# Kernel tuning notes

Measured on AMD Instinct MI355X. Metric: run time of the kernel, lower is better.

Reference implementation:

```python
import jax, jax.numpy as jnp
import numpy as np

N_NODES = 50000
N_EDGES = 800000
IN, HID, OUT = 128, 32, 64
HEADS = (4, 4, 4, 4)  # heads per layer (heads[0], heads[1], heads[1], heads[2])
NEG_SLOPE = 0.2


def gat_layer(h, src, dst, W, al, ar, b, activation):
    """One DGL-style GATConv. h: [N, Din]; W: [Din, H*F]; al, ar: [H, F]; b: [H*F]."""
    n = h.shape[0]
    H, F = al.shape
    feat = (h @ W).reshape(n, H, F)                       # [N, H, F]
    el = jnp.sum(feat * al, axis=-1)                      # [N, H]
    er = jnp.sum(feat * ar, axis=-1)                      # [N, H]
    e = jax.nn.leaky_relu(el[src] + er[dst], NEG_SLOPE)   # [E, H]
    # segment softmax over incoming edges of each dst node
    m = jax.ops.segment_max(e, dst, num_segments=n)       # [N, H]
    ex = jnp.exp(e - m[dst])                              # [E, H]
    denom = jax.ops.segment_sum(ex, dst, num_segments=n)  # [N, H]
    alpha = ex / jnp.maximum(denom[dst], 1e-9)            # [E, H]
    msg = feat[src] * alpha[:, :, None]                   # [E, H, F]
    out = jax.ops.segment_sum(msg, dst, num_segments=n) + b.reshape(H, F)
    return activation(out) if activation is not None else out


def setup_inputs() -> dict:
    key = jax.random.key(0)
    ks = jax.random.split(key, 20)
    x = jax.random.normal(ks[0], (N_NODES, IN), dtype=jnp.float32)
    src = jax.random.randint(ks[1], (N_EDGES,), 0, N_NODES, dtype=jnp.int32)
    dst = jax.random.randint(ks[2], (N_EDGES,), 0, N_NODES, dtype=jnp.int32)
    dims = [(IN, HEADS[0], HID), (HID * HEADS[0], HEADS[1], HID),
            (HID * HEADS[1], HEADS[2], HID), (HID * HEADS[2], HEADS[3], OUT)]
    inp = {"x": x, "src": src, "dst": dst}
    k = 3
    for i, (din, h, f) in enumerate(dims, start=1):
        inp[f"W{i}"] = jax.random.normal(ks[k], (din, h * f), dtype=jnp.float32) * 0.05; k += 1
        inp[f"al{i}"] = jax.random.normal(ks[k], (h, f), dtype=jnp.float32) * 0.05; k += 1
        inp[f"ar{i}"] = jax.random.normal(ks[k], (h, f), dtype=jnp.float32) * 0.05; k += 1
        inp[f"b{i}"] = jnp.zeros((h * f,), dtype=jnp.float32)
    return inp


def reference(x, src, dst, W1, al1, ar1, b1, W2, al2, ar2, b2,
              W3, al3, ar3, b3, W4, al4, ar4, b4):
    elu = jax.nn.elu
    h = gat_layer(x, src, dst, W1, al1, ar1, b1, elu).reshape(N_NODES, -1)   # flatten heads
    h = gat_layer(h, src, dst, W2, al2, ar2, b2, elu).reshape(N_NODES, -1)
    h = gat_layer(h, src, dst, W3, al3, ar3, b3, elu).reshape(N_NODES, -1)
    h = gat_layer(h, src, dst, W4, al4, ar4, b4, None).mean(axis=1)          # mean over heads
    return h
```

## Files before the change

### kernel.cpp

```cpp
#include <hip/hip_runtime.h>
#include <hip/hip_fp16.h>

#define N_NODES 50000
#define N_EDGES 800000

typedef _Float16 h8 __attribute__((ext_vector_type(8)));
typedef float f4 __attribute__((ext_vector_type(4)));

__device__ __forceinline__ float lrelu(float x){ return x > 0.f ? x : 0.2f*x; }
__device__ __forceinline__ float eluf (float x){ return x > 0.f ? x : __expf(x)-1.f; }

__global__ void k_histwt(const int* __restrict__ dst, int* __restrict__ cnt,
                         const float* __restrict__ W1, const float* __restrict__ W2,
                         const float* __restrict__ W3, const float* __restrict__ W4,
                         _Float16* __restrict__ wt){
  int b = blockIdx.x;
  if (b < 3125){
    int e = b*256 + threadIdx.x;
    if (e < N_EDGES) atomicAdd(&cnt[dst[e]], 1);
  } else {
    int id = (b - 3125)*256 + threadIdx.x;
    if (id < 81920){
      const float* W; int HF; int loc;
      if (id < 16384)      { W = W1; HF = 128; loc = id; }
      else if (id < 32768) { W = W2; HF = 128; loc = id - 16384; }
      else if (id < 49152) { W = W3; HF = 128; loc = id - 32768; }
      else                 { W = W4; HF = 256; loc = id - 49152; }
      int n = loc >> 7, k = loc & 127;
      wt[id] = (_Float16)W[(size_t)k*HF + n];
    }
  }
}

__global__ void k_scan1(const int* __restrict__ cnt, int* __restrict__ offs, int* __restrict__ bsum){
  __shared__ int tmp[256];
  int tid = threadIdx.x; int i = blockIdx.x*256 + tid;
  int v = (i < N_NODES) ? cnt[i] : 0;
  tmp[tid] = v; __syncthreads();
  for (int d = 1; d < 256; d <<= 1){
    int t = (tid >= d) ? tmp[tid-d] : 0;
    __syncthreads();
    tmp[tid] += t;
    __syncthreads();
  }
  if (i < N_NODES) offs[i] = tmp[tid] - v;
  if (tid == 255) bsum[blockIdx.x] = tmp[tid];
}

__global__ void k_scan2(int* __restrict__ bsum, int nb){
  __shared__ int tmp[256];
  int tid = threadIdx.x;
  int v = (tid < nb) ? bsum[tid] : 0;
  tmp[tid] = v; __syncthreads();
  for (int d = 1; d < 256; d <<= 1){
    int t = (tid >= d) ? tmp[tid-d] : 0;
    __syncthreads();
    tmp[tid] += t;
    __syncthreads();
  }
  if (tid < nb) bsum[tid] = tmp[tid] - v;
}

__global__ void k_scan3(int* __restrict__ offs, const int* __restrict__ bsum, int* __restrict__ cur){
  int i = blockIdx.x*256 + threadIdx.x;
  if (i < N_NODES){
    int o = offs[i] + bsum[blockIdx.x];
    offs[i] = o; cur[i] = o;
  }
  if (i == 0) offs[N_NODES] = N_EDGES;
}

__global__ void k_scatter(const int* __restrict__ src, const int* __restrict__ dst,
                          int* __restrict__ cur, int* __restrict__ csr_src){
  int e = blockIdx.x*256 + threadIdx.x;
  if (e < N_EDGES){
    int pos = atomicAdd(&cur[dst[e]], 1);
    csr_src[pos] = src[e];
  }
}

template<int HF, bool AHALF>
__global__ __launch_bounds__(256) void k_gemm(const void* __restrict__ Ain,
        const _Float16* __restrict__ Wt,
        __half* __restrict__ feat,
        const float* __restrict__ al, const float* __restrict__ ar,
        float* __restrict__ el, float* __restrict__ er){
  __shared__ char lds[49152];
  char* Alds = lds;
  char* Blds = lds + 32768;
  _Float16* Clds = (_Float16*)lds;
  const int tid  = threadIdx.x;
  const int row0 = blockIdx.x * 128;
  const int col0 = blockIdx.y * 64;

  if (AHALF){
    const __half* A16 = (const __half*)Ain;
    #pragma unroll
    for (int i = 0; i < 8; ++i){
      int flat = i*256 + tid;
      int r = flat >> 4, ch = flat & 15;
      uint4 v = make_uint4(0,0,0,0);
      if (row0 + r < N_NODES) v = *(const uint4*)&A16[(size_t)(row0+r)*128 + ch*8];
      *(uint4*)(Alds + ((r*256 + ch*16) ^ ((r&7)<<4))) = v;
    }
  } else {
    const float* A32 = (const float*)Ain;
    #pragma unroll
    for (int i = 0; i < 8; ++i){
      int flat = i*256 + tid;
      int r = flat >> 4, ch = flat & 15;
      h8 hv = {};
      if (row0 + r < N_NODES){
        float4 f0 = *(const float4*)&A32[(size_t)(row0+r)*128 + ch*8];
        float4 f1 = *(const float4*)&A32[(size_t)(row0+r)*128 + ch*8 + 4];
        hv[0]=(_Float16)f0.x; hv[1]=(_Float16)f0.y; hv[2]=(_Float16)f0.z; hv[3]=(_Float16)f0.w;
        hv[4]=(_Float16)f1.x; hv[5]=(_Float16)f1.y; hv[6]=(_Float16)f1.z; hv[7]=(_Float16)f1.w;
      }
      *(h8*)(Alds + ((r*256 + ch*16) ^ ((r&7)<<4))) = hv;
    }
  }
  #pragma unroll
  for (int i = 0; i < 4; ++i){
    int flat = i*256 + tid;
    int n = flat >> 4, ch = flat & 15;
    uint4 v = *(const uint4*)&Wt[(size_t)(col0+n)*128 + ch*8];
    *(uint4*)(Blds + ((n*256 + ch*16) ^ ((n&7)<<4))) = v;
  }
  __syncthreads();

  const int l = tid & 63, w = tid >> 6;
  f4 acc[2][4] = {};
  const int rA0  = w*32 + (l & 15);
  const int rA1  = rA0 + 16;
  const int nB   = (l & 15);
  const int ksel = (l >> 4) * 16;
  #pragma unroll
  for (int kb = 0; kb < 4; ++kb){
    int kofs = kb*64 + ksel;
    h8 a0 = *(const h8*)(Alds + ((rA0*256 + kofs) ^ ((rA0&7)<<4)));
    h8 a1 = *(const h8*)(Alds + ((rA1*256 + kofs) ^ ((rA1&7)<<4)));
    h8 b[4];
    #pragma unroll
    for (int nf = 0; nf < 4; ++nf){
      int n = nB + nf*16;
      b[nf] = *(const h8*)(Blds + ((n*256 + kofs) ^ ((n&7)<<4)));
    }
    #pragma unroll
    for (int nf = 0; nf < 4; ++nf){
      acc[0][nf] = __builtin_amdgcn_mfma_f32_16x16x32_f16(a0, b[nf], acc[0][nf], 0, 0, 0);
      acc[1][nf] = __builtin_amdgcn_mfma_f32_16x16x32_f16(a1, b[nf], acc[1][nf], 0, 0, 0);
    }
  }
  __syncthreads();

  #pragma unroll
  for (int mf = 0; mf < 2; ++mf){
    int rloc = w*32 + mf*16 + (l>>4)*4;
    #pragma unroll
    for (int nf = 0; nf < 4; ++nf){
      int c = nf*16 + (l&15);
      #pragma unroll
      for (int reg = 0; reg < 4; ++reg)
        Clds[(rloc+reg)*80 + c] = (_Float16)acc[mf][nf][reg];
    }
  }
  __syncthreads();

  constexpr int F = HF/4;
  int ch = l & 7;
  float4 al0 = *(const float4*)&al[col0 + ch*8];
  float4 al1 = *(const float4*)&al[col0 + ch*8 + 4];
  float4 ar0 = *(const float4*)&ar[col0 + ch*8];
  float4 ar1 = *(const float4*)&ar[col0 + ch*8 + 4];
  #pragma unroll
  for (int i = 0; i < 4; ++i){
    int rloc = i*32 + w*8 + (l>>3);
    int grow = row0 + rloc;
    h8 hv = *(const h8*)&Clds[rloc*80 + ch*8];
    if (grow < N_NODES)
      *(uint4*)&feat[(size_t)grow*HF + col0 + ch*8] = *(uint4*)&hv;
    float f0=(float)hv[0], f1=(float)hv[1], f2=(float)hv[2], f3=(float)hv[3];
    float f4_=(float)hv[4], f5=(float)hv[5], f6=(float)hv[6], f7=(float)hv[7];
    float pl = f0*al0.x + f1*al0.y + f2*al0.z + f3*al0.w
             + f4_*al1.x + f5*al1.y + f6*al1.z + f7*al1.w;
    float pr = f0*ar0.x + f1*ar0.y + f2*ar0.z + f3*ar0.w
             + f4_*ar1.x + f5*ar1.y + f6*ar1.z + f7*ar1.w;
    pl += __shfl_xor(pl, 1); pl += __shfl_xor(pl, 2);
    pr += __shfl_xor(pr, 1); pr += __shfl_xor(pr, 2);
    if (F == 64){ pl += __shfl_xor(pl, 4); pr += __shfl_xor(pr, 4); }
    bool lead = (F == 32) ? ((l & 3) == 0) : ((l & 7) == 0);
    if (lead && grow < N_NODES){
      int h = (col0 + ch*8) / F;
      el[grow*4 + h] = pl;
      er[grow*4 + h] = pr;
    }
  }
}

template<int F, bool FINAL, int LAYER>
__global__ __launch_bounds__(256) void k_agg(const int* __restrict__ offs,
        const int* __restrict__ csr_src, const float* __restrict__ el,
        const float* __restrict__ er, const __half* __restrict__ feat,
        const float* __restrict__ bias, void* __restrict__ out){
  __shared__ float s_ev[4][64][4];
  __shared__ int   s_src[4][64];
  int tid  = threadIdx.x;
  int wv   = tid >> 6;
  int lane = tid & 63;
  int n = blockIdx.x*4 + wv;
  int beg = offs[n], end = offs[n+1];
  float4 er4 = ((const float4*)er)[n];

  if (F == 32){
    int quarter = lane >> 4;
    int l4      = lane & 15;
    int h       = l4 >> 2;
    float a0=0.f,a1=0.f,a2=0.f,a3=0.f,a4=0.f,a5=0.f,a6=0.f,a7=0.f,ds=0.f;
    for (int cbeg = beg; cbeg < end; cbeg += 64){
      int m = end - cbeg; if (m > 64) m = 64;
      if (lane < m){
        int s = csr_src[cbeg + lane];
        s_src[wv][lane] = s;
        float4 e4 = *(const float4*)&el[(size_t)s*4];
        float4 ev4;
        ev4.x = __expf(lrelu(e4.x + er4.x));
        ev4.y = __expf(lrelu(e4.y + er4.y));
        ev4.z = __expf(lrelu(e4.z + er4.z));
        ev4.w = __expf(lrelu(e4.w + er4.w));
        *(float4*)&s_ev[wv][lane][0] = ev4;
      }
      asm volatile("s_waitcnt lgkmcnt(0)" ::: "memory");
      #pragma unroll 4
      for (int i = 0; i < m; i += 4){
        int e = i + quarter;
        if (e < m){
          int s = s_src[wv][e];
          float w = s_ev[wv][e][h];
          ds += w;
          uint4 raw = *(const uint4*)&feat[(size_t)s*128 + l4*8];
          const __half2* hp = reinterpret_cast<const __half2*>(&raw);
          float2 f0 = __half22float2(hp[0]);
          float2 f1 = __half22float2(hp[1]);
          float2 f2 = __half22float2(hp[2]);
          float2 f3 = __half22float2(hp[3]);
          a0 += w*f0.x; a1 += w*f0.y; a2 += w*f1.x; a3 += w*f1.y;
          a4 += w*f2.x; a5 += w*f2.y; a6 += w*f3.x; a7 += w*f3.y;
        }
      }
      asm volatile("" ::: "memory");
    }
    ds += __shfl_xor(ds, 16); ds += __shfl_xor(ds, 32);
    a0 += __shfl_xor(a0, 16); a0 += __shfl_xor(a0, 32);
    a1 += __shfl_xor(a1, 16); a1 += __shfl_xor(a1, 32);
    a2 += __shfl_xor(a2, 16); a2 += __shfl_xor(a2, 32);
    a3 += __shfl_xor(a3, 16); a3 += __shfl_xor(a3, 32);
    a4 += __shfl_xor(a4, 16); a4 += __shfl_xor(a4, 32);
    a5 += __shfl_xor(a5, 16); a5 += __shfl_xor(a5, 32);
    a6 += __shfl_xor(a6, 16); a6 += __shfl_xor(a6, 32);
    a7 += __shfl_xor(a7, 16); a7 += __shfl_xor(a7, 32);
    if (quarter == 0){
      float rden = 1.f / fmaxf(ds, 1e-9f);
      float4 b0 = *(const float4*)&bias[l4*8];
      float4 b1 = *(const float4*)&bias[l4*8 + 4];
      float o0 = eluf(a0*rden + b0.x);
      float o1 = eluf(a1*rden + b0.y);
      float o2 = eluf(a2*rden + b0.z);
      float o3 = eluf(a3*rden + b0.w);
      float o4 = eluf(a4*rden + b1.x);
      float o5 = eluf(a5*rden + b1.y);
      float o6 = eluf(a6*rden + b1.z);
      float o7 = eluf(a7*rden + b1.w);
      __half* outh = (__half*)out;
      h8 hv;
      hv[0]=(_Float16)o0; hv[1]=(_Float16)o1; hv[2]=(_Float16)o2; hv[3]=(_Float16)o3;
      hv[4]=(_Float16)o4; hv[5]=(_Float16)o5; hv[6]=(_Float16)o6; hv[7]=(_Float16)o7;
      *(uint4*)&outh[(size_t)n*128 + l4*8] = *(uint4*)&hv;
    }
  } else {
    int hw  = lane >> 5;
    int l5  = lane & 31;
    int h   = l5 >> 3;
    float a0=0.f,a1=0.f,a2=0.f,a3=0.f,a4=0.f,a5=0.f,a6=0.f,a7=0.f,ds=0.f;
    for (int cbeg = beg; cbeg < end; cbeg += 64){
      int m = end - cbeg; if (m > 64) m = 64;
      if (lane < m){
        int s = csr_src[cbeg + lane];
        s_src[wv][lane] = s;
        float4 e4 = *(const float4*)&el[(size_t)s*4];
        float4 ev4;
        ev4.x = __expf(lrelu(e4.x + er4.x));
        ev4.y = __expf(lrelu(e4.y + er4.y));
        ev4.z = __expf(lrelu(e4.z + er4.z));
        ev4.w = __expf(lrelu(e4.w + er4.w));
        *(float4*)&s_ev[wv][lane][0] = ev4;
      }
      asm volatile("s_waitcnt lgkmcnt(0)" ::: "memory");
      #pragma unroll 4
      for (int i = 0; i < m; i += 2){
        int e = i + hw;
        if (e < m){
          int s = s_src[wv][e];
          float w = s_ev[wv][e][h];
          ds += w;
          uint4 raw = *(const uint4*)&feat[(size_t)s*256 + l5*8];
          const __half2* hp = reinterpret_cast<const __half2*>(&raw);
          float2 f0 = __half22float2(hp[0]);
          float2 f1 = __half22float2(hp[1]);
          float2 f2 = __half22float2(hp[2]);
          float2 f3 = __half22float2(hp[3]);
          a0 += w*f0.x; a1 += w*f0.y; a2 += w*f1.x; a3 += w*f1.y;
          a4 += w*f2.x; a5 += w*f2.y; a6 += w*f3.x; a7 += w*f3.y;
        }
      }
      asm volatile("" ::: "memory");
    }
    ds += __shfl_xor(ds, 32);
    a0 += __shfl_xor(a0, 32); a1 += __shfl_xor(a1, 32);
    a2 += __shfl_xor(a2, 32); a3 += __shfl_xor(a3, 32);
    a4 += __shfl_xor(a4, 32); a5 += __shfl_xor(a5, 32);
    a6 += __shfl_xor(a6, 32); a7 += __shfl_xor(a7, 32);
    float rden = 1.f / fmaxf(ds, 1e-9f);
    float4 b0 = *(const float4*)&bias[l5*8];
    float4 b1 = *(const float4*)&bias[l5*8 + 4];
    float v0 = a0*rden + b0.x;
    float v1 = a1*rden + b0.y;
    float v2 = a2*rden + b0.z;
    float v3 = a3*rden + b0.w;
    float v4 = a4*rden + b1.x;
    float v5 = a5*rden + b1.y;
    float v6 = a6*rden + b1.z;
    float v7 = a7*rden + b1.w;
    v0 += __shfl_xor(v0, 8); v0 += __shfl_xor(v0, 16);
    v1 += __shfl_xor(v1, 8); v1 += __shfl_xor(v1, 16);
    v2 += __shfl_xor(v2, 8); v2 += __shfl_xor(v2, 16);
    v3 += __shfl_xor(v3, 8); v3 += __shfl_xor(v3, 16);
    v4 += __shfl_xor(v4, 8); v4 += __shfl_xor(v4, 16);
    v5 += __shfl_xor(v5, 8); v5 += __shfl_xor(v5, 16);
    v6 += __shfl_xor(v6, 8); v6 += __shfl_xor(v6, 16);
    v7 += __shfl_xor(v7, 8); v7 += __shfl_xor(v7, 16);
    if (hw == 0 && l5 < 8){
      float* outf = (float*)out;
      *(float4*)&outf[(size_t)n*64 + l5*8] =
        make_float4(v0*0.25f, v1*0.25f, v2*0.25f, v3*0.25f);
      *(float4*)&outf[(size_t)n*64 + l5*8 + 4] =
        make_float4(v4*0.25f, v5*0.25f, v6*0.25f, v7*0.25f);
    }
  }
}

extern "C" void kernel_launch(void* const* d_in, const int* in_sizes, int n_in,
                              void* d_out, int out_size, void* d_ws, size_t ws_size,
                              hipStream_t stream){
  const float* x   = (const float*)d_in[0];
  const int*   src = (const int*)  d_in[1];
  const int*   dst = (const int*)  d_in[2];
  const float* W[4]  = {(const float*)d_in[3],  (const float*)d_in[7],
                        (const float*)d_in[11], (const float*)d_in[15]};
  const float* al[4] = {(const float*)d_in[4],  (const float*)d_in[8],
                        (const float*)d_in[12], (const float*)d_in[16]};
  const float* ar[4] = {(const float*)d_in[5],  (const float*)d_in[9],
                        (const float*)d_in[13], (const float*)d_in[17]};
  const float* b[4]  = {(const float*)d_in[6],  (const float*)d_in[10],
                        (const float*)d_in[14], (const float*)d_in[18]};

  char* ws = (char*)d_ws;
  __half*    bufH    = (__half*)   (ws);
  __half*    feat    = (__half*)   (ws + 25600000);
  _Float16*  wt      = (_Float16*) (ws + 51200000);
  float*     el      = (float*)    (ws + 76800000);
  float*     er      = (float*)    (ws + 77600000);
  int*       offs    = (int*)      (ws + 78400000);
  int*       cur     = (int*)      (ws + 78600032);
  int*       bsum    = (int*)      (ws + 78800032);
  int*       csr_src = (int*)      (ws + 78801056);

  (void)hipMemsetAsync(cur, 0, N_NODES*sizeof(int), stream);
  k_histwt <<<3445, 256, 0, stream>>>(dst, cur, W[0], W[1], W[2], W[3], wt);
  k_scan1  <<<196,  256, 0, stream>>>(cur, offs, bsum);
  k_scan2  <<<1,    256, 0, stream>>>(bsum, 196);
  k_scan3  <<<196,  256, 0, stream>>>(offs, bsum, cur);
  k_scatter<<<3125, 256, 0, stream>>>(src, dst, cur, csr_src);

  k_gemm<128,false><<<dim3(391,2), 256, 0, stream>>>(x, wt, feat, al[0], ar[0], el, er);
  k_agg<32,false,1><<<12500, 256, 0, stream>>>(offs, csr_src, el, er, feat, b[0], bufH);

  k_gemm<128,true><<<dim3(391,2), 256, 0, stream>>>(bufH, wt + 16384, feat, al[1], ar[1], el, er);
  k_agg<32,false,2><<<12500, 256, 0, stream>>>(offs, csr_src, el, er, feat, b[1], bufH);

  k_gemm<128,true><<<dim3(391,2), 256, 0, stream>>>(bufH, wt + 32768, feat, al[2], ar[2], el, er);
  k_agg<32,false,3><<<12500, 256, 0, stream>>>(offs, csr_src, el, er, feat, b[2], bufH);

  k_gemm<256,true><<<dim3(391,4), 256, 0, stream>>>(bufH, wt + 49152, feat, al[3], ar[3], el, er);
  k_agg<64,true,4><<<12500, 256, 0, stream>>>(offs, csr_src, el, er, feat, b[3], d_out);
}
```

Measured before the change: 432.0 us.

## Split hidden-layer aggregation across heads with a per-head grid dimension

```diff
diff --git a/kernel.cpp b/kernel.cpp
--- a/kernel.cpp
+++ b/kernel.cpp
@@ -197,6 +197,78 @@
   }
 }
 
+template<int LAYER>
+__global__ __launch_bounds__(256) void k_aggh(const int* __restrict__ offs,
+        const int* __restrict__ csr_src, const float* __restrict__ el,
+        const float* __restrict__ er, const __half* __restrict__ feat,
+        const float* __restrict__ bias, __half* __restrict__ out){
+  __shared__ float s_ev[4][64];
+  __shared__ int   s_src[4][64];
+  int tid  = threadIdx.x;
+  int wv   = tid >> 6;
+  int lane = tid & 63;
+  int h    = blockIdx.y;
+  int n    = blockIdx.x*4 + wv;
+  int beg = offs[n], end = offs[n+1];
+  float er_h = er[n*4 + h];
+  int eg = lane >> 2;
+  int fq = lane & 3;
+  float a0=0.f,a1=0.f,a2=0.f,a3=0.f,a4=0.f,a5=0.f,a6=0.f,a7=0.f,ds=0.f;
+
+  for (int cbeg = beg; cbeg < end; cbeg += 64){
+    int m = end - cbeg; if (m > 64) m = 64;
+    if (lane < m){
+      int s = csr_src[cbeg + lane];
+      s_src[wv][lane] = s;
+      s_ev[wv][lane] = __expf(lrelu(el[s*4 + h] + er_h));
+    }
+    asm volatile("s_waitcnt lgkmcnt(0)" ::: "memory");
+    #pragma unroll 2
+    for (int i = 0; i < m; i += 16){
+      int e = i + eg;
+      if (e < m){
+        int s = s_src[wv][e];
+        float w = s_ev[wv][e];
+        ds += w;
+        uint4 raw = *(const uint4*)&feat[(size_t)s*128 + h*32 + fq*8];
+        const __half2* hp = reinterpret_cast<const __half2*>(&raw);
+        float2 f0 = __half22float2(hp[0]);
+        float2 f1 = __half22float2(hp[1]);
+        float2 f2 = __half22float2(hp[2]);
+        float2 f3 = __half22float2(hp[3]);
+        a0 += w*f0.x; a1 += w*f0.y; a2 += w*f1.x; a3 += w*f1.y;
+        a4 += w*f2.x; a5 += w*f2.y; a6 += w*f3.x; a7 += w*f3.y;
+      }
+    }
+    asm volatile("" ::: "memory");
+  }
+  #pragma unroll
+  for (int msk = 4; msk < 64; msk <<= 1){
+    ds += __shfl_xor(ds, msk);
+    a0 += __shfl_xor(a0, msk); a1 += __shfl_xor(a1, msk);
+    a2 += __shfl_xor(a2, msk); a3 += __shfl_xor(a3, msk);
+    a4 += __shfl_xor(a4, msk); a5 += __shfl_xor(a5, msk);
+    a6 += __shfl_xor(a6, msk); a7 += __shfl_xor(a7, msk);
+  }
+  if (eg == 0){
+    float rden = 1.f / fmaxf(ds, 1e-9f);
+    float4 b0 = *(const float4*)&bias[h*32 + fq*8];
+    float4 b1 = *(const float4*)&bias[h*32 + fq*8 + 4];
+    float o0 = eluf(a0*rden + b0.x);
+    float o1 = eluf(a1*rden + b0.y);
+    float o2 = eluf(a2*rden + b0.z);
+    float o3 = eluf(a3*rden + b0.w);
+    float o4 = eluf(a4*rden + b1.x);
+    float o5 = eluf(a5*rden + b1.y);
+    float o6 = eluf(a6*rden + b1.z);
+    float o7 = eluf(a7*rden + b1.w);
+    h8 hv;
+    hv[0]=(_Float16)o0; hv[1]=(_Float16)o1; hv[2]=(_Float16)o2; hv[3]=(_Float16)o3;
+    hv[4]=(_Float16)o4; hv[5]=(_Float16)o5; hv[6]=(_Float16)o6; hv[7]=(_Float16)o7;
+    *(uint4*)&out[(size_t)n*128 + h*32 + fq*8] = *(uint4*)&hv;
+  }
+}
+
 template<int F, bool FINAL, int LAYER>
 __global__ __launch_bounds__(256) void k_agg(const int* __restrict__ offs,
         const int* __restrict__ csr_src, const float* __restrict__ el,
@@ -211,140 +283,73 @@
   int beg = offs[n], end = offs[n+1];
   float4 er4 = ((const float4*)er)[n];
 
-  if (F == 32){
-    int quarter = lane >> 4;
-    int l4      = lane & 15;
-    int h       = l4 >> 2;
-    float a0=0.f,a1=0.f,a2=0.f,a3=0.f,a4=0.f,a5=0.f,a6=0.f,a7=0.f,ds=0.f;
-    for (int cbeg = beg; cbeg < end; cbeg += 64){
-      int m = end - cbeg; if (m > 64) m = 64;
-      if (lane < m){
-        int s = csr_src[cbeg + lane];
-        s_src[wv][lane] = s;
-        float4 e4 = *(const float4*)&el[(size_t)s*4];
-        float4 ev4;
-        ev4.x = __expf(lrelu(e4.x + er4.x));
-        ev4.y = __expf(lrelu(e4.y + er4.y));
-        ev4.z = __expf(lrelu(e4.z + er4.z));
-        ev4.w = __expf(lrelu(e4.w + er4.w));
-        *(float4*)&s_ev[wv][lane][0] = ev4;
+  int hw  = lane >> 5;
+  int l5  = lane & 31;
+  int h   = l5 >> 3;
+  float a0=0.f,a1=0.f,a2=0.f,a3=0.f,a4=0.f,a5=0.f,a6=0.f,a7=0.f,ds=0.f;
+  for (int cbeg = beg; cbeg < end; cbeg += 64){
+    int m = end - cbeg; if (m > 64) m = 64;
+    if (lane < m){
+      int s = csr_src[cbeg + lane];
+      s_src[wv][lane] = s;
+      float4 e4 = *(const float4*)&el[(size_t)s*4];
+      float4 ev4;
+      ev4.x = __expf(lrelu(e4.x + er4.x));
+      ev4.y = __expf(lrelu(e4.y + er4.y));
+      ev4.z = __expf(lrelu(e4.z + er4.z));
+      ev4.w = __expf(lrelu(e4.w + er4.w));
+      *(float4*)&s_ev[wv][lane][0] = ev4;
+    }
+    asm volatile("s_waitcnt lgkmcnt(0)" ::: "memory");
+    #pragma unroll 4
+    for (int i = 0; i < m; i += 2){
+      int e = i + hw;
+      if (e < m){
+        int s = s_src[wv][e];
+        float w = s_ev[wv][e][h];
+        ds += w;
+        uint4 raw = *(const uint4*)&feat[(size_t)s*256 + l5*8];
+        const __half2* hp = reinterpret_cast<const __half2*>(&raw);
+        float2 f0 = __half22float2(hp[0]);
+        float2 f1 = __half22float2(hp[1]);
+        float2 f2 = __half22float2(hp[2]);
+        float2 f3 = __half22float2(hp[3]);
+        a0 += w*f0.x; a1 += w*f0.y; a2 += w*f1.x; a3 += w*f1.y;
+        a4 += w*f2.x; a5 += w*f2.y; a6 += w*f3.x; a7 += w*f3.y;
       }
-      asm volatile("s_waitcnt lgkmcnt(0)" ::: "memory");
-      #pragma unroll 4
-      for (int i = 0; i < m; i += 4){
-        int e = i + quarter;
-        if (e < m){
-          int s = s_src[wv][e];
-          float w = s_ev[wv][e][h];
-          ds += w;
-          uint4 raw = *(const uint4*)&feat[(size_t)s*128 + l4*8];
-          const __half2* hp = reinterpret_cast<const __half2*>(&raw);
-          float2 f0 = __half22float2(hp[0]);
-          float2 f1 = __half22float2(hp[1]);
-          float2 f2 = __half22float2(hp[2]);
-          float2 f3 = __half22float2(hp[3]);
-          a0 += w*f0.x; a1 += w*f0.y; a2 += w*f1.x; a3 += w*f1.y;
-          a4 += w*f2.x; a5 += w*f2.y; a6 += w*f3.x; a7 += w*f3.y;
-        }
-      }
-      asm volatile("" ::: "memory");
-    }
-    ds += __shfl_xor(ds, 16); ds += __shfl_xor(ds, 32);
-    a0 += __shfl_xor(a0, 16); a0 += __shfl_xor(a0, 32);
-    a1 += __shfl_xor(a1, 16); a1 += __shfl_xor(a1, 32);
-    a2 += __shfl_xor(a2, 16); a2 += __shfl_xor(a2, 32);
-    a3 += __shfl_xor(a3, 16); a3 += __shfl_xor(a3, 32);
-    a4 += __shfl_xor(a4, 16); a4 += __shfl_xor(a4, 32);
-    a5 += __shfl_xor(a5, 16); a5 += __shfl_xor(a5, 32);
-    a6 += __shfl_xor(a6, 16); a6 += __shfl_xor(a6, 32);
-    a7 += __shfl_xor(a7, 16); a7 += __shfl_xor(a7, 32);
-    if (quarter == 0){
-      float rden = 1.f / fmaxf(ds, 1e-9f);
-      float4 b0 = *(const float4*)&bias[l4*8];
-      float4 b1 = *(const float4*)&bias[l4*8 + 4];
-      float o0 = eluf(a0*rden + b0.x);
-      float o1 = eluf(a1*rden + b0.y);
-      float o2 = eluf(a2*rden + b0.z);
-      float o3 = eluf(a3*rden + b0.w);
-      float o4 = eluf(a4*rden + b1.x);
-      float o5 = eluf(a5*rden + b1.y);
-      float o6 = eluf(a6*rden + b1.z);
-      float o7 = eluf(a7*rden + b1.w);
-      __half* outh = (__half*)out;
-      h8 hv;
-      hv[0]=(_Float16)o0; hv[1]=(_Float16)o1; hv[2]=(_Float16)o2; hv[3]=(_Float16)o3;
-      hv[4]=(_Float16)o4; hv[5]=(_Float16)o5; hv[6]=(_Float16)o6; hv[7]=(_Float16)o7;
-      *(uint4*)&outh[(size_t)n*128 + l4*8] = *(uint4*)&hv;
-    }
-  } else {
-    int hw  = lane >> 5;
-    int l5  = lane & 31;
-    int h   = l5 >> 3;
-    float a0=0.f,a1=0.f,a2=0.f,a3=0.f,a4=0.f,a5=0.f,a6=0.f,a7=0.f,ds=0.f;
-    for (int cbeg = beg; cbeg < end; cbeg += 64){
-      int m = end - cbeg; if (m > 64) m = 64;
-      if (lane < m){
-        int s = csr_src[cbeg + lane];
-        s_src[wv][lane] = s;
-        float4 e4 = *(const float4*)&el[(size_t)s*4];
-        float4 ev4;
-        ev4.x = __expf(lrelu(e4.x + er4.x));
-        ev4.y = __expf(lrelu(e4.y + er4.y));
-        ev4.z = __expf(lrelu(e4.z + er4.z));
-        ev4.w = __expf(lrelu(e4.w + er4.w));
-        *(float4*)&s_ev[wv][lane][0] = ev4;
-      }
-      asm volatile("s_waitcnt lgkmcnt(0)" ::: "memory");
-      #pragma unroll 4
-      for (int i = 0; i < m; i += 2){
-        int e = i + hw;
-        if (e < m){
-          int s = s_src[wv][e];
-          float w = s_ev[wv][e][h];
-          ds += w;
-          uint4 raw = *(const uint4*)&feat[(size_t)s*256 + l5*8];
-          const __half2* hp = reinterpret_cast<const __half2*>(&raw);
-          float2 f0 = __half22float2(hp[0]);
-          float2 f1 = __half22float2(hp[1]);
-          float2 f2 = __half22float2(hp[2]);
-          float2 f3 = __half22float2(hp[3]);
-          a0 += w*f0.x; a1 += w*f0.y; a2 += w*f1.x; a3 += w*f1.y;
-          a4 += w*f2.x; a5 += w*f2.y; a6 += w*f3.x; a7 += w*f3.y;
-        }
-      }
-      asm volatile("" ::: "memory");
-    }
-    ds += __shfl_xor(ds, 32);
-    a0 += __shfl_xor(a0, 32); a1 += __shfl_xor(a1, 32);
-    a2 += __shfl_xor(a2, 32); a3 += __shfl_xor(a3, 32);
-    a4 += __shfl_xor(a4, 32); a5 += __shfl_xor(a5, 32);
-    a6 += __shfl_xor(a6, 32); a7 += __shfl_xor(a7, 32);
-    float rden = 1.f / fmaxf(ds, 1e-9f);
-    float4 b0 = *(const float4*)&bias[l5*8];
-    float4 b1 = *(const float4*)&bias[l5*8 + 4];
-    float v0 = a0*rden + b0.x;
-    float v1 = a1*rden + b0.y;
-    float v2 = a2*rden + b0.z;
-    float v3 = a3*rden + b0.w;
-    float v4 = a4*rden + b1.x;
-    float v5 = a5*rden + b1.y;
-    float v6 = a6*rden + b1.z;
-    float v7 = a7*rden + b1.w;
-    v0 += __shfl_xor(v0, 8); v0 += __shfl_xor(v0, 16);
-    v1 += __shfl_xor(v1, 8); v1 += __shfl_xor(v1, 16);
-    v2 += __shfl_xor(v2, 8); v2 += __shfl_xor(v2, 16);
-    v3 += __shfl_xor(v3, 8); v3 += __shfl_xor(v3, 16);
-    v4 += __shfl_xor(v4, 8); v4 += __shfl_xor(v4, 16);
-    v5 += __shfl_xor(v5, 8); v5 += __shfl_xor(v5, 16);
-    v6 += __shfl_xor(v6, 8); v6 += __shfl_xor(v6, 16);
-    v7 += __shfl_xor(v7, 8); v7 += __shfl_xor(v7, 16);
-    if (hw == 0 && l5 < 8){
-      float* outf = (float*)out;
-      *(float4*)&outf[(size_t)n*64 + l5*8] =
-        make_float4(v0*0.25f, v1*0.25f, v2*0.25f, v3*0.25f);
-      *(float4*)&outf[(size_t)n*64 + l5*8 + 4] =
-        make_float4(v4*0.25f, v5*0.25f, v6*0.25f, v7*0.25f);
-    }
+    }
+    asm volatile("" ::: "memory");
+  }
+  ds += __shfl_xor(ds, 32);
+  a0 += __shfl_xor(a0, 32); a1 += __shfl_xor(a1, 32);
+  a2 += __shfl_xor(a2, 32); a3 += __shfl_xor(a3, 32);
+  a4 += __shfl_xor(a4, 32); a5 += __shfl_xor(a5, 32);
+  a6 += __shfl_xor(a6, 32); a7 += __shfl_xor(a7, 32);
+  float rden = 1.f / fmaxf(ds, 1e-9f);
+  float4 b0 = *(const float4*)&bias[l5*8];
+  float4 b1 = *(const float4*)&bias[l5*8 + 4];
+  float v0 = a0*rden + b0.x;
+  float v1 = a1*rden + b0.y;
+  float v2 = a2*rden + b0.z;
+  float v3 = a3*rden + b0.w;
+  float v4 = a4*rden + b1.x;
+  float v5 = a5*rden + b1.y;
+  float v6 = a6*rden + b1.z;
+  float v7 = a7*rden + b1.w;
+  v0 += __shfl_xor(v0, 8); v0 += __shfl_xor(v0, 16);
+  v1 += __shfl_xor(v1, 8); v1 += __shfl_xor(v1, 16);
+  v2 += __shfl_xor(v2, 8); v2 += __shfl_xor(v2, 16);
+  v3 += __shfl_xor(v3, 8); v3 += __shfl_xor(v3, 16);
+  v4 += __shfl_xor(v4, 8); v4 += __shfl_xor(v4, 16);
+  v5 += __shfl_xor(v5, 8); v5 += __shfl_xor(v5, 16);
+  v6 += __shfl_xor(v6, 8); v6 += __shfl_xor(v6, 16);
+  v7 += __shfl_xor(v7, 8); v7 += __shfl_xor(v7, 16);
+  if (hw == 0 && l5 < 8){
+    float* outf = (float*)out;
+    *(float4*)&outf[(size_t)n*64 + l5*8] =
+      make_float4(v0*0.25f, v1*0.25f, v2*0.25f, v3*0.25f);
+    *(float4*)&outf[(size_t)n*64 + l5*8 + 4] =
+      make_float4(v4*0.25f, v5*0.25f, v6*0.25f, v7*0.25f);
   }
 }
 
@@ -382,13 +387,13 @@
   k_scatter<<<3125, 256, 0, stream>>>(src, dst, cur, csr_src);
 
   k_gemm<128,false><<<dim3(391,2), 256, 0, stream>>>(x, wt, feat, al[0], ar[0], el, er);
-  k_agg<32,false,1><<<12500, 256, 0, stream>>>(offs, csr_src, el, er, feat, b[0], bufH);
+  k_aggh<1><<<dim3(12500,4), 256, 0, stream>>>(offs, csr_src, el, er, feat, b[0], bufH);
 
   k_gemm<128,true><<<dim3(391,2), 256, 0, stream>>>(bufH, wt + 16384, feat, al[1], ar[1], el, er);
-  k_agg<32,false,2><<<12500, 256, 0, stream>>>(offs, csr_src, el, er, feat, b[1], bufH);
+  k_aggh<2><<<dim3(12500,4), 256, 0, stream>>>(offs, csr_src, el, er, feat, b[1], bufH);
 
   k_gemm<128,true><<<dim3(391,2), 256, 0, stream>>>(bufH, wt + 32768, feat, al[2], ar[2], el, er);
-  k_agg<32,false,3><<<12500, 256, 0, stream>>>(offs, csr_src, el, er, feat, b[2], bufH);
+  k_aggh<3><<<dim3(12500,4), 256, 0, stream>>>(offs, csr_src, el, er, feat, b[2], bufH);
 
   k_gemm<256,true><<<dim3(391,4), 256, 0, stream>>>(bufH, wt + 49152, feat, al[3], ar[3], el, er);
   k_agg<64,true,4><<<12500, 256, 0, stream>>>(offs, csr_src, el, er, feat, b[3], d_out);
```

New measurement: 588.5 us. 36.2% more time.
